# Kernel tuning notes

Measured on AMD Instinct MI355X. Metric: run time of the kernel, lower is better.

Reference implementation:

```python
import jax, jax.numpy as jnp
import numpy as np

E, H, D = 512, 8, 64
B, T = 2, 1024
HD = H * D


def _linear(x, W, b):
    return x @ W + b


def _ln(x, g, b):
    mu = x.mean(-1, keepdims=True)
    var = ((x - mu) ** 2).mean(-1, keepdims=True)
    return (x - mu) / jnp.sqrt(var + 1e-5) * g + b


def _l2norm(x):
    n = jnp.sqrt((x * x).sum(-1, keepdims=True))
    return x / jnp.maximum(n, 1e-12)


def setup_inputs() -> dict:
    key = jax.random.key(0)
    ks = jax.random.split(key, 32)
    s = 0.02
    inp = {
        'x': jax.random.normal(ks[0], (B, T, E), jnp.float32),
        'b_min': jax.random.normal(ks[1], (B, T, E), jnp.float32),
        'b_max': jax.random.normal(ks[2], (B, T, E), jnp.float32),
        'motif_context': jax.random.normal(ks[3], (B, T, E), jnp.float32),
        'Wk': jax.random.normal(ks[4], (E, HD), jnp.float32) * s,
        'bk': jnp.zeros((HD,), jnp.float32),
        'Wq': jax.random.normal(ks[5], (E, HD), jnp.float32) * s,
        'bq': jnp.zeros((HD,), jnp.float32),
        'Wv': jax.random.normal(ks[6], (E, HD), jnp.float32) * s,
        'bv': jnp.zeros((HD,), jnp.float32),
        'Wo': jax.random.normal(ks[7], (HD, E), jnp.float32) * s,
        'bo': jnp.zeros((E,), jnp.float32),
        'Wd': jax.random.normal(ks[8], (E, H), jnp.float32) * s,
        'bd': jnp.zeros((H,), jnp.float32),
        'Wgw': jax.random.normal(ks[9], (E, H), jnp.float32) * s,
        'bgw': jnp.zeros((H,), jnp.float32),
        'Wgf': jax.random.normal(ks[10], (E, H), jnp.float32) * s,
        'bgf': jnp.zeros((H,), jnp.float32),
        'Wps': jax.random.normal(ks[11], (E, E), jnp.float32) * s,
        'bps': jnp.zeros((E,), jnp.float32),
        'ln1_g': jnp.ones((E,), jnp.float32),
        'ln1_b': jnp.zeros((E,), jnp.float32),
        'ln2_g': jnp.ones((E,), jnp.float32),
        'ln2_b': jnp.zeros((E,), jnp.float32),
        'W1': jax.random.normal(ks[12], (E, 4 * E), jnp.float32) * s,
        'b1': jnp.zeros((4 * E,), jnp.float32),
        'W2': jax.random.normal(ks[13], (4 * E, E), jnp.float32) * s,
        'b2': jnp.zeros((E,), jnp.float32),
    }
    return inp


def reference(x, b_min, b_max, motif_context,
              Wk, bk, Wq, bq, Wv, bv, Wo, bo, Wd, bd,
              Wgw, bgw, Wgf, bgf, Wps, bps,
              ln1_g, ln1_b, ln2_g, ln2_b, W1, b1, W2, b2):
    Bs, Ts, Es = x.shape
    x_n = _ln(x, ln1_g, ln1_b)
    k = _l2norm(_linear(x_n, Wk, bk).reshape(Bs, Ts, H, D))
    q = _l2norm(_linear(x_n, Wq, bq).reshape(Bs, Ts, H, D))
    v = jnp.tanh(_linear(x_n, Wv, bv).reshape(Bs, Ts, H, D))
    d = jax.nn.softplus(_linear(x_n, Wd, bd))            # (B,T,H)
    gw = jax.nn.sigmoid(_linear(x_n, Wgw, bgw)) ** 2     # (B,T,H)
    gf = 1.0 - jax.nn.sigmoid(_linear(x_n, Wgf, bgf)) ** 2

    # gated linear recurrent scan via cumsum of rank-1 updates
    v_gated = v * (d * gw)[..., None]                    # (B,T,H,D)
    updates = jnp.einsum('bthi,bthj->bthij', v_gated, k)  # (B,T,H,D,D)
    decay = jnp.clip(d * gf, 1e-6, 0.999)
    log_decay = jnp.log(decay)[..., None, None]          # (B,T,H,1,1)
    exp_cum_decay = jnp.exp(jnp.cumsum(log_decay, axis=1))
    state = jnp.cumsum(updates / (exp_cum_decay + 1e-8), axis=1) * exp_cum_decay
    readout = jnp.einsum('bthij,bthj->bthi', state, q)   # (B,T,H,D)
    next_mem = state[:, -1]

    x2 = x + _linear(readout.reshape(Bs, Ts, HD), Wo, bo) + 0.1 * motif_context
    h = _ln(x2, ln2_g, ln2_b)
    x3 = x2 + _linear(jax.nn.gelu(_linear(h, W1, b1), approximate=False), W2, b2)
    probe = _linear(x3, Wps, bps)
    return (x3, next_mem, b_min + probe, b_max + probe)
```

## Files before the change

kernel.cpp:

```cpp
#include <hip/hip_runtime.h>


typedef unsigned short u16;
typedef unsigned int u32;
typedef __attribute__((ext_vector_type(8))) short short8;
typedef __attribute__((ext_vector_type(4))) float floatx4;

__device__ __forceinline__ float b2f(u16 u) {
  u32 x = ((u32)u) << 16;
  return __uint_as_float(x);
}
__device__ __forceinline__ u16 f2b(float f) {
  u32 x = __float_as_uint(f);
  u32 r = (x + 0x7fffu + ((x >> 16) & 1u)) >> 16;
  return (u16)r;
}
__device__ __forceinline__ float4 b4_to_f4(uint2 u) {
  float4 r;
  r.x = __uint_as_float((u.x & 0xffffu) << 16);
  r.y = __uint_as_float(u.x & 0xffff0000u);
  r.z = __uint_as_float((u.y & 0xffffu) << 16);
  r.w = __uint_as_float(u.y & 0xffff0000u);
  return r;
}

__device__ __forceinline__ void stage16(const u16* g, u16* lds_wave_base) {
  __builtin_amdgcn_global_load_lds((const __attribute__((address_space(1))) void*)g,
                                   (__attribute__((address_space(3))) void*)lds_wave_base,
                                   16, 0, 0);
}

template <int ROWS>
__device__ __forceinline__ void stage_tile64(const u16* __restrict__ G, int ldK, int kb,
                                             u16* lds, int tid) {
#pragma unroll
  for (int r = 0; r < ROWS / 32; ++r) {
    int slot = r * 256 + tid;
    int row = slot >> 3;
    int kwg = (slot & 7) ^ (row & 7);
    stage16(G + (size_t)row * ldK + kb * 64 + kwg * 8,
            lds + (size_t)(r * 256 + (tid >> 6) * 64) * 8);
  }
}

__device__ __forceinline__ void ln_row(const float* __restrict__ xr,
                                       const float* __restrict__ g,
                                       const float* __restrict__ bt,
                                       u16* __restrict__ yr, int tid, float* red) {
  float x0 = xr[tid], x1 = xr[tid + 256];
  float s = x0 + x1, ss = x0 * x0 + x1 * x1;
#pragma unroll
  for (int o = 32; o > 0; o >>= 1) { s += __shfl_xor(s, o); ss += __shfl_xor(ss, o); }
  if ((tid & 63) == 0) { red[tid >> 6] = s; red[4 + (tid >> 6)] = ss; }
  __syncthreads();
  float ts = red[0] + red[1] + red[2] + red[3];
  float tss = red[4] + red[5] + red[6] + red[7];
  float mu = ts * (1.f / 512.f);
  float var = tss * (1.f / 512.f) - mu * mu;
  float rstd = 1.0f / sqrtf(var + 1e-5f);
  yr[tid] = f2b((x0 - mu) * rstd * g[tid] + bt[tid]);
  yr[tid + 256] = f2b((x1 - mu) * rstd * g[tid + 256] + bt[tid + 256]);
}

__global__ __launch_bounds__(256) void prep_weights(
    const float* __restrict__ Wk, const float* __restrict__ Wq,
    const float* __restrict__ Wv, const float* __restrict__ Wo,
    const float* __restrict__ Wps, const float* __restrict__ W1,
    const float* __restrict__ W2, const float* __restrict__ Wd,
    const float* __restrict__ Wgw, const float* __restrict__ Wgf,
    const float* __restrict__ bk, const float* __restrict__ bq,
    const float* __restrict__ bv, const float* __restrict__ bd,
    const float* __restrict__ bgw, const float* __restrict__ bgf,
    const float* __restrict__ x, const float* __restrict__ ln1g,
    const float* __restrict__ ln1b,
    u16* __restrict__ WTQ, u16* __restrict__ WTO, u16* __restrict__ WTPS,
    u16* __restrict__ WT1, u16* __restrict__ WT2, float* __restrict__ BQV,
    u16* __restrict__ XN) {
  int bid = blockIdx.x, tid = threadIdx.x;
  __shared__ float tile[32][33];
  __shared__ float red[8];
#pragma unroll 1
  for (int rep = 0; rep < 3; ++rep) {
    __syncthreads();
    if (bid < 3328) {
      const float* src;
      u16* dst;
      int C, rel, tiles_x;
      if (bid < 256)       { src = Wk;  dst = WTQ;           C = 512;  rel = bid;        tiles_x = 16; }
      else if (bid < 512)  { src = Wq;  dst = WTQ + 262144;  C = 512;  rel = bid - 256;  tiles_x = 16; }
      else if (bid < 768)  { src = Wv;  dst = WTQ + 524288;  C = 512;  rel = bid - 512;  tiles_x = 16; }
      else if (bid < 1024) { src = Wo;  dst = WTO;           C = 512;  rel = bid - 768;  tiles_x = 16; }
      else if (bid < 1280) { src = Wps; dst = WTPS;          C = 512;  rel = bid - 1024; tiles_x = 16; }
      else if (bid < 2304) { src = W1;  dst = WT1;           C = 2048; rel = bid - 1280; tiles_x = 64; }
      else                 { src = W2;  dst = WT2;           C = 512;  rel = bid - 2304; tiles_x = 16; }
      int R = (bid >= 1280 && bid < 2304) ? 512 : (bid >= 2304 ? 2048 : 512);
      int c0 = (rel % tiles_x) * 32, r0 = (rel / tiles_x) * 32;
      int tx = tid & 31, ty = tid >> 5;
#pragma unroll
      for (int i = 0; i < 4; ++i)
        tile[ty + i * 8][tx] = src[(size_t)(r0 + ty + i * 8) * C + c0 + tx];
      __syncthreads();
#pragma unroll
      for (int i = 0; i < 4; ++i)
        dst[(size_t)(c0 + ty + i * 8) * R + r0 + tx] = f2b(tile[tx][ty + i * 8]);
    } else if (bid < 3392) {
      int idx = (bid - 3328) * 256 + tid;
      const int stride = 64 * 256;
      for (int i = idx; i < 128 * 512; i += stride) {
        int local = i >> 9, k = i & 511;
        float v = 0.f;
        if (local < 8) v = Wd[k * 8 + local];
        else if (local < 16) v = Wgw[k * 8 + (local - 8)];
        else if (local < 24) v = Wgf[k * 8 + (local - 16)];
        WTQ[(size_t)(1536 + local) * 512 + k] = f2b(v);
      }
      for (int i = idx; i < 1664; i += stride) {
        float v = 0.f;
        if (i < 512) v = bk[i];
        else if (i < 1024) v = bq[i - 512];
        else if (i < 1536) v = bv[i - 1024];
        else if (i < 1544) v = bd[i - 1536];
        else if (i < 1552) v = bgw[i - 1544];
        else if (i < 1560) v = bgf[i - 1552];
        BQV[i] = v;
      }
    } else {
      int row = bid - 3392;
      ln_row(x + (size_t)row * 512, ln1g, ln1b, XN + (size_t)row * 512, tid, red);
    }
  }
}

__global__ __launch_bounds__(256) void ln_f32(const float* __restrict__ X,
                                              const float* __restrict__ g,
                                              const float* __restrict__ bt,
                                              u16* __restrict__ Y) {
  __shared__ float red[8];
#pragma unroll 1
  for (int rep = 0; rep < 3; ++rep) {
    __syncthreads();
    ln_row(X + (size_t)blockIdx.x * 512, g, bt, Y + (size_t)blockIdx.x * 512,
           threadIdx.x, red);
  }
}

template <int BM, int EPI>
__global__ __launch_bounds__(256, 4) void gemm2s(
    const u16* __restrict__ A, const u16* __restrict__ BT, const float* __restrict__ bias,
    float* __restrict__ outf, float* __restrict__ outf2, u16* __restrict__ outb,
    u16* __restrict__ outb2, u16* __restrict__ outb3,
    const float* __restrict__ aux0, const float* __restrict__ aux1, int M, int N, int K) {
  constexpr int MT = BM / 32;
  constexpr int S = BM / 32 + 2;
  constexpr int STAGES = (BM == 32 ? 3 : 2);
  __shared__ __align__(16) u16 As[STAGES][BM * 64];
  __shared__ __align__(16) u16 Bs[STAGES][64 * 64];
  __shared__ float ssb[2][BM];
  const int tid = threadIdx.x;
  const int lane = tid & 63, wave = tid >> 6;
  const int wm = wave >> 1, wn = wave & 1;
  const int m0 = blockIdx.y * BM, n0 = blockIdx.x * 64;
  floatx4 acc[MT][2] = {};
  const int fr = lane & 15, kq = lane >> 4;
  const int nk = K >> 6;
  const u16* Ab = A + (size_t)m0 * K;
  const u16* Bb = BT + (size_t)n0 * K;

  stage_tile64<BM>(Ab, K, 0, As[0], tid);
  stage_tile64<64>(Bb, K, 0, Bs[0], tid);
  if constexpr (STAGES == 3) {
    if (nk > 1) {
      stage_tile64<BM>(Ab, K, 1, As[1], tid);
      stage_tile64<64>(Bb, K, 1, Bs[1], tid);
    }
  }

  for (int kb = 0; kb < nk; ++kb) {
    const int cur = kb % STAGES;
    if (kb + STAGES - 1 < nk) {
      const int nxt = (kb + STAGES - 1) % STAGES;
      stage_tile64<BM>(Ab, K, kb + STAGES - 1, As[nxt], tid);
      stage_tile64<64>(Bb, K, kb + STAGES - 1, Bs[nxt], tid);
    }
    if constexpr (STAGES == 3) {
      if (kb + 2 < nk) asm volatile("s_waitcnt vmcnt(6)" ::: "memory");
      else if (kb + 1 < nk) asm volatile("s_waitcnt vmcnt(3)" ::: "memory");
      else asm volatile("s_waitcnt vmcnt(0)" ::: "memory");
    } else {
      if (kb + 1 < nk) {
        if constexpr (S == 4) asm volatile("s_waitcnt vmcnt(4)" ::: "memory");
        else asm volatile("s_waitcnt vmcnt(3)" ::: "memory");
      } else {
        asm volatile("s_waitcnt vmcnt(0)" ::: "memory");
      }
    }
    asm volatile("s_barrier" ::: "memory");

#pragma unroll
    for (int sub = 0; sub < 2; ++sub) {
      short8 af[MT], bf[2];
#pragma unroll
      for (int mt = 0; mt < MT; ++mt) {
        int row = wm * (BM / 2) + mt * 16 + fr;
        int c = sub * 4 + kq;
        af[mt] = *(const short8*)&As[cur][row * 64 + ((c ^ (row & 7)) << 3)];
      }
#pragma unroll
      for (int nt = 0; nt < 2; ++nt) {
        int row = wn * 32 + nt * 16 + fr;
        int c = sub * 4 + kq;
        bf[nt] = *(const short8*)&Bs[cur][row * 64 + ((c ^ (row & 7)) << 3)];
      }
#pragma unroll
      for (int mt = 0; mt < MT; ++mt)
#pragma unroll
        for (int nt = 0; nt < 2; ++nt)
          acc[mt][nt] =
              __builtin_amdgcn_mfma_f32_16x16x32_bf16(af[mt], bf[nt], acc[mt][nt], 0, 0, 0);
    }
    asm volatile("s_waitcnt lgkmcnt(0)" ::: "memory");
    asm volatile("s_barrier" ::: "memory");
  }

  const int col = lane & 15;
  const int rbase = (lane >> 4) * 4;

  float vv[MT][2][4];
#pragma unroll
  for (int nt = 0; nt < 2; ++nt) {
    int gc = n0 + wn * 32 + nt * 16 + col;
    float bvv = bias[gc];
#pragma unroll
    for (int mt = 0; mt < MT; ++mt)
#pragma unroll
      for (int r = 0; r < 4; ++r) vv[mt][nt][r] = acc[mt][nt][r] + bvv;
  }

  if constexpr (EPI == 5) {
    const int sec = n0 >> 9;
    const int h = (n0 & 511) >> 6;
    if (sec == 3) {
#pragma unroll
      for (int nt = 0; nt < 2; ++nt) {
        int gcl = (n0 - 1536) + wn * 32 + nt * 16 + col;
#pragma unroll
        for (int mt = 0; mt < MT; ++mt) {
          int gr = m0 + wm * (BM / 2) + mt * 16 + rbase;
#pragma unroll
          for (int r = 0; r < 4; ++r)
            outf[(size_t)(gr + r) * 128 + gcl] = vv[mt][nt][r];
        }
      }
    } else if (sec == 2) {
#pragma unroll
      for (int nt = 0; nt < 2; ++nt) {
        int d = wn * 32 + nt * 16 + col;
#pragma unroll
        for (int mt = 0; mt < MT; ++mt) {
          int gr = m0 + wm * (BM / 2) + mt * 16 + rbase;
#pragma unroll
          for (int r = 0; r < 4; ++r) {
            int tok = gr + r;
            int bh = (tok >> 10) * 8 + h;
            outb3[((size_t)bh * 1024 + (tok & 1023)) * 64 + d] = f2b(tanhf(vv[mt][nt][r]));
          }
        }
      }
    } else {
#pragma unroll
      for (int mt = 0; mt < MT; ++mt) {
#pragma unroll
        for (int r = 0; r < 4; ++r) {
          float ss = vv[mt][0][r] * vv[mt][0][r] + vv[mt][1][r] * vv[mt][1][r];
          ss += __shfl_xor(ss, 1);
          ss += __shfl_xor(ss, 2);
          ss += __shfl_xor(ss, 4);
          ss += __shfl_xor(ss, 8);
          if ((lane & 15) == 0)
            ssb[wn][wm * (BM / 2) + mt * 16 + rbase + r] = ss;
        }
      }
      __syncthreads();
      u16* dst = (sec == 0) ? outb : outb2;
#pragma unroll
      for (int mt = 0; mt < MT; ++mt) {
#pragma unroll
        for (int r = 0; r < 4; ++r) {
          int br = wm * (BM / 2) + mt * 16 + rbase + r;
          float tot = ssb[0][br] + ssb[1][br];
          float rs = 1.0f / fmaxf(sqrtf(tot), 1e-12f);
          int tok = m0 + br;
          int bh = (tok >> 10) * 8 + h;
          size_t base = ((size_t)bh * 1024 + (tok & 1023)) * 64;
#pragma unroll
          for (int nt = 0; nt < 2; ++nt) {
            int d = wn * 32 + nt * 16 + col;
            dst[base + d] = f2b(vv[mt][nt][r] * rs);
          }
        }
      }
    }
  } else {
#pragma unroll
    for (int nt = 0; nt < 2; ++nt) {
      int gc = n0 + wn * 32 + nt * 16 + col;
#pragma unroll
      for (int mt = 0; mt < MT; ++mt) {
        int gr = m0 + wm * (BM / 2) + mt * 16 + rbase;
#pragma unroll
        for (int r = 0; r < 4; ++r) {
          size_t idx = (size_t)(gr + r) * N + gc;
          float v = vv[mt][nt][r];
          if constexpr (EPI == 1) {
            outf[idx] = aux0[idx] + v + 0.1f * aux1[idx];
          } else if constexpr (EPI == 2) {
            outb[idx] = f2b(0.5f * v * (1.f + erff(v * 0.70710678118654752f)));
          } else if constexpr (EPI == 3) {
            float w = aux0[idx] + v;
            outf[idx] = w;
            outb[idx] = f2b(w);
          } else if constexpr (EPI == 4) {
            outf[idx] = aux0[idx] + v;
            outf2[idx] = aux1[idx] + v;
          }
        }
      }
    }
  }
}

__global__ __launch_bounds__(256) void gates_logcum(
    const float* __restrict__ G0, float* __restrict__ DEC, float* __restrict__ WS,
    float* __restrict__ LC) {
  int bh = blockIdx.x;
  int b = bh >> 3, h = bh & 7;
  int tid = threadIdx.x;
  __shared__ float ldec[1024];
  __shared__ float lsvg[1024];
#pragma unroll 1
  for (int rep = 0; rep < 3; ++rep) {
    __syncthreads();
#pragma unroll
    for (int tt = 0; tt < 4; ++tt) {
      int t = tt * 256 + tid;
      size_t tok = (size_t)b * 1024 + t;
      float dl = G0[tok * 128 + h];
      float gwl = G0[tok * 128 + 8 + h];
      float gfl = G0[tok * 128 + 16 + h];
      float dd = dl > 20.f ? dl : log1pf(expf(dl));
      float sw = 1.f / (1.f + expf(-gwl));
      float gw = sw * sw;
      float sf = 1.f / (1.f + expf(-gfl));
      float gf = 1.f - sf * sf;
      float dec = fminf(fmaxf(dd * gf, 1e-6f), 0.999f);
      ldec[t] = dec;
      lsvg[t] = dd * gw;
      DEC[(size_t)bh * 1024 + t] = dec;
    }
    __syncthreads();
    if (tid < 64) {
      int lane = tid;
      size_t base = (size_t)bh * 1024 + lane * 16;
      float loc[16];
      float run = 0.f;
#pragma unroll
      for (int i = 0; i < 16; ++i) { run += logf(ldec[lane * 16 + i]); loc[i] = run; }
      float x = run;
#pragma unroll
      for (int o = 1; o < 64; o <<= 1) {
        float v = __shfl_up(x, o);
        if (lane >= o) x += v;
      }
      float excl = x - run;
#pragma unroll
      for (int i = 0; i < 16; ++i) {
        float L = excl + loc[i];
        LC[base + i] = L;
        float c = expf(L);
        WS[base + i] = (c / (c + 1e-8f)) * lsvg[lane * 16 + i];
      }
    }
  }
}

__global__ __launch_bounds__(256, 2) void scan_phase1(
    const u16* __restrict__ KB, const u16* __restrict__ QB, const u16* __restrict__ VB,
    const float* __restrict__ DEC, const float* __restrict__ WS,
    float* __restrict__ RP, float* __restrict__ SF) {
  int chunk = blockIdx.x, h = blockIdx.y, b = blockIdx.z;
  int bh = b * 8 + h;
  int t0 = chunk * 32;
  __shared__ __align__(16) float sk[2048], sq[2048], sv[2048];
  __shared__ float lsa[32], lsw[32];
  int tid = threadIdx.x;

#pragma unroll 1
  for (int rep = 0; rep < 3; ++rep) {
    __syncthreads();
    const u16* gk = KB + ((size_t)bh * 1024 + t0) * 64;
    const u16* gq = QB + ((size_t)bh * 1024 + t0) * 64;
    const u16* gv = VB + ((size_t)bh * 1024 + t0) * 64;
#pragma unroll
    for (int r = 0; r < 2; ++r) {
      int f = (r * 256 + tid) * 4;
      *(float4*)&sk[f] = b4_to_f4(*(const uint2*)(gk + f));
      *(float4*)&sq[f] = b4_to_f4(*(const uint2*)(gq + f));
      *(float4*)&sv[f] = b4_to_f4(*(const uint2*)(gv + f));
    }
    if (tid < 32) {
      size_t gi = (size_t)bh * 1024 + t0 + tid;
      lsa[tid] = DEC[gi];
      lsw[tid] = WS[gi];
    }
    __syncthreads();

    int i = tid >> 2, j0 = (tid & 3) * 16;
    float s[16];
#pragma unroll
    for (int z = 0; z < 16; ++z) s[z] = 0.f;

    for (int t = 0; t < 32; ++t) {
      float a = lsa[t], w = lsw[t];
      float wv = w * sv[t * 64 + i];
      float r = 0.f;
#pragma unroll
      for (int u4 = 0; u4 < 4; ++u4) {
        float4 kv = *(const float4*)&sk[t * 64 + j0 + u4 * 4];
        float4 qv = *(const float4*)&sq[t * 64 + j0 + u4 * 4];
        s[u4 * 4 + 0] = fmaf(a, s[u4 * 4 + 0], wv * kv.x); r = fmaf(s[u4 * 4 + 0], qv.x, r);
        s[u4 * 4 + 1] = fmaf(a, s[u4 * 4 + 1], wv * kv.y); r = fmaf(s[u4 * 4 + 1], qv.y, r);
        s[u4 * 4 + 2] = fmaf(a, s[u4 * 4 + 2], wv * kv.z); r = fmaf(s[u4 * 4 + 2], qv.z, r);
        s[u4 * 4 + 3] = fmaf(a, s[u4 * 4 + 3], wv * kv.w); r = fmaf(s[u4 * 4 + 3], qv.w, r);
      }
      r += __shfl_xor(r, 1);
      r += __shfl_xor(r, 2);
      if ((tid & 3) == 0)
        RP[((size_t)(b * 1024 + t0 + t) * 8 + h) * 64 + i] = r;
    }

    float* Sf = SF + ((size_t)bh * 32 + chunk) * 4096 + i * 64 + j0;
#pragma unroll
    for (int u4 = 0; u4 < 4; ++u4) {
      float4 v;
      v.x = s[u4 * 4 + 0]; v.y = s[u4 * 4 + 1]; v.z = s[u4 * 4 + 2]; v.w = s[u4 * 4 + 3];
      *(float4*)&Sf[u4 * 4] = v;
    }
  }
}

__global__ __launch_bounds__(256) void scan_phase2p(const float* __restrict__ SF,
                                                    const float* __restrict__ LC,
                                                    float* __restrict__ SI,
                                                    float* __restrict__ next_mem) {
  int bh = blockIdx.x >> 4;
  int e = (blockIdx.x & 15) * 256 + threadIdx.x;
#pragma unroll 1
  for (int rep = 0; rep < 3; ++rep) {
    float s = 0.f;
    for (int c = 0; c < 32; ++c) {
      SI[((size_t)bh * 32 + c) * 4096 + e] = s;
      float Lend = LC[(size_t)bh * 1024 + c * 32 + 31];
      float Lpre = c ? LC[(size_t)bh * 1024 + c * 32 - 1] : 0.f;
      float P = expf(Lend - Lpre);
      s = fmaf(P, s, SF[((size_t)bh * 32 + c) * 4096 + e]);
    }
    next_mem[(size_t)bh * 4096 + e] = s;
  }
}

__global__ __launch_bounds__(256, 2) void scan_phase3(
    const u16* __restrict__ QB, const float* __restrict__ SI, const float* __restrict__ LC,
    const float* __restrict__ RP, u16* __restrict__ AB) {
  int chunk = blockIdx.x, h = blockIdx.y, b = blockIdx.z;
  int bh = b * 8 + h;
  int t0 = chunk * 32;
  __shared__ __align__(16) float sq[2048];
  __shared__ float sL[32];
  int tid = threadIdx.x;

#pragma unroll 1
  for (int rep = 0; rep < 3; ++rep) {
    __syncthreads();
    const u16* gq = QB + ((size_t)bh * 1024 + t0) * 64;
#pragma unroll
    for (int r = 0; r < 2; ++r) {
      int f = (r * 256 + tid) * 4;
      *(float4*)&sq[f] = b4_to_f4(*(const uint2*)(gq + f));
    }
    if (tid < 32) sL[tid] = LC[(size_t)bh * 1024 + t0 + tid];
    __syncthreads();

    float Lpre = chunk ? LC[(size_t)bh * 1024 + t0 - 1] : 0.f;
    int i = tid >> 2, j0 = (tid & 3) * 16;
    const float* Si = SI + ((size_t)bh * 32 + chunk) * 4096 + i * 64 + j0;
    float S[16];
#pragma unroll
    for (int u4 = 0; u4 < 4; ++u4) {
      float4 v = *(const float4*)&Si[u4 * 4];
      S[u4 * 4 + 0] = v.x; S[u4 * 4 + 1] = v.y; S[u4 * 4 + 2] = v.z; S[u4 * 4 + 3] = v.w;
    }

    for (int t = 0; t < 32; ++t) {
      float p = expf(sL[t] - Lpre);
      float r = 0.f;
#pragma unroll
      for (int u4 = 0; u4 < 4; ++u4) {
        float4 qv = *(const float4*)&sq[t * 64 + j0 + u4 * 4];
        r = fmaf(S[u4 * 4 + 0], qv.x, r);
        r = fmaf(S[u4 * 4 + 1], qv.y, r);
        r = fmaf(S[u4 * 4 + 2], qv.z, r);
        r = fmaf(S[u4 * 4 + 3], qv.w, r);
      }
      r += __shfl_xor(r, 1);
      r += __shfl_xor(r, 2);
      if ((tid & 3) == 0) {
        size_t gi = ((size_t)(b * 1024 + t0 + t) * 8 + h) * 64 + i;
        AB[gi] = f2b(RP[gi] + p * r);
      }
    }
  }
}

extern "C" void kernel_launch(void* const* d_in, const int* in_sizes, int n_in,
                              void* d_out, int out_size, void* d_ws, size_t ws_size,
                              hipStream_t stream) {
  const float* x = (const float*)d_in[0];
  const float* bmin = (const float*)d_in[1];
  const float* bmax = (const float*)d_in[2];
  const float* motif = (const float*)d_in[3];
  const float* Wk = (const float*)d_in[4];
  const float* bk = (const float*)d_in[5];
  const float* Wq = (const float*)d_in[6];
  const float* bq = (const float*)d_in[7];
  const float* Wv = (const float*)d_in[8];
  const float* bv = (const float*)d_in[9];
  const float* Wo = (const float*)d_in[10];
  const float* bo = (const float*)d_in[11];
  const float* Wd = (const float*)d_in[12];
  const float* bd = (const float*)d_in[13];
  const float* Wgw = (const float*)d_in[14];
  const float* bgw = (const float*)d_in[15];
  const float* Wgf = (const float*)d_in[16];
  const float* bgf = (const float*)d_in[17];
  const float* Wps = (const float*)d_in[18];
  const float* bps = (const float*)d_in[19];
  const float* ln1g = (const float*)d_in[20];
  const float* ln1b = (const float*)d_in[21];
  const float* ln2g = (const float*)d_in[22];
  const float* ln2b = (const float*)d_in[23];
  const float* W1 = (const float*)d_in[24];
  const float* b1 = (const float*)d_in[25];
  const float* W2 = (const float*)d_in[26];
  const float* b2 = (const float*)d_in[27];

  char* ws = (char*)d_ws;
  u16* WTQ = (u16*)(ws + 0);
  u16* WTO = (u16*)(ws + 1703936);
  u16* WT1 = (u16*)(ws + 2228224);
  u16* WT2 = (u16*)(ws + 4325376);
  u16* WTPS = (u16*)(ws + 6422528);
  float* BQV = (float*)(ws + 6946816);
  u16* XN = (u16*)(ws + 6953984);
  float* G0 = (float*)(ws + 9051136);
  u16* KB = (u16*)(ws + 10099712);
  u16* QB = (u16*)(ws + 12196864);
  u16* VB = (u16*)(ws + 14294016);
  float* DEC = (float*)(ws + 16391168);
  float* LC = (float*)(ws + 16456704);
  float* WS = (float*)(ws + 16522240);
  float* RP = (float*)(ws + 16653312);
  float* SF = (float*)(ws + 20847616);
  float* SI = (float*)(ws + 29236224);
  u16* AB = (u16*)(ws + 37624832);
  float* X2 = (float*)(ws + 39721984);
  u16* HB = (u16*)(ws + 43916288);
  u16* MID = (u16*)(ws + 9051136);
  u16* X3B = (u16*)(ws + 20847616);

  float* out0 = (float*)d_out;
  float* out1 = out0 + 1048576;
  float* out2 = out0 + 1114112;
  float* out3 = out0 + 2162688;

  prep_weights<<<5440, 256, 0, stream>>>(Wk, Wq, Wv, Wo, Wps, W1, W2, Wd, Wgw, Wgf,
                                         bk, bq, bv, bd, bgw, bgf, x, ln1g, ln1b,
                                         WTQ, WTO, WTPS, WT1, WT2, BQV, XN);
  gemm2s<64, 5><<<dim3(26, 32), 256, 0, stream>>>(XN, WTQ, BQV, G0, nullptr, KB, QB, VB,
                                                  nullptr, nullptr, 2048, 1664, 512);
  gates_logcum<<<16, 256, 0, stream>>>(G0, DEC, WS, LC);
  scan_phase1<<<dim3(32, 8, 2), 256, 0, stream>>>(KB, QB, VB, DEC, WS, RP, SF);
  scan_phase2p<<<256, 256, 0, stream>>>(SF, LC, SI, out1);
  scan_phase3<<<dim3(32, 8, 2), 256, 0, stream>>>(QB, SI, LC, RP, AB);

  gemm2s<32, 1><<<dim3(8, 64), 256, 0, stream>>>(AB, WTO, bo, X2, nullptr, nullptr,
                                                 nullptr, nullptr, x, motif, 2048, 512, 512);
  ln_f32<<<2048, 256, 0, stream>>>(X2, ln2g, ln2b, HB);
  gemm2s<64, 2><<<dim3(32, 32), 256, 0, stream>>>(HB, WT1, b1, nullptr, nullptr, MID,
                                                  nullptr, nullptr, nullptr, nullptr,
                                                  2048, 2048, 512);
  gemm2s<32, 3><<<dim3(8, 64), 256, 0, stream>>>(MID, WT2, b2, out0, nullptr, X3B,
                                                 nullptr, nullptr, X2, nullptr,
                                                 2048, 512, 2048);
  gemm2s<32, 4><<<dim3(8, 64), 256, 0, stream>>>(X3B, WTPS, bps, out2, out3, nullptr,
                                                 nullptr, nullptr, bmin, bmax,
                                                 2048, 512, 512);
}
```

Before: 279.6 us.

## Fold LN2 into W1 GEMM epilogue and drop redundant repeat loops

Removes the standalone ln_f32 kernel. The Wo GEMM epilogue now writes x2 in both fp32 and bf16 and accumulates per-row sum and sum-of-squares with atomics. The W1 GEMM applies the normalisation algebraically, using ln2_g folded into the transposed W1 and precomputed column vectors U1 and V1. It also deletes the triple-repeat loops in the prep, gates, scan and LN kernels, which redid identical work three times. The trade-offs are atomics in the epilogue, a variance computed as E[x^2]-mu^2, and GEMM input that is x2 rounded to bf16 before normalisation instead of after.

```diff
diff --git a/kernel.cpp b/kernel.cpp
--- a/kernel.cpp
+++ b/kernel.cpp
@@ -72,75 +72,74 @@
     const float* __restrict__ bv, const float* __restrict__ bd,
     const float* __restrict__ bgw, const float* __restrict__ bgf,
     const float* __restrict__ x, const float* __restrict__ ln1g,
-    const float* __restrict__ ln1b,
+    const float* __restrict__ ln1b, const float* __restrict__ ln2g,
+    const float* __restrict__ ln2b, const float* __restrict__ b1v,
     u16* __restrict__ WTQ, u16* __restrict__ WTO, u16* __restrict__ WTPS,
     u16* __restrict__ WT1, u16* __restrict__ WT2, float* __restrict__ BQV,
-    u16* __restrict__ XN) {
+    u16* __restrict__ XN, float* __restrict__ U1, float* __restrict__ V1,
+    float* __restrict__ RS) {
   int bid = blockIdx.x, tid = threadIdx.x;
   __shared__ float tile[32][33];
   __shared__ float red[8];
-#pragma unroll 1
-  for (int rep = 0; rep < 3; ++rep) {
+  if (bid < 3328) {
+    const float* src;
+    u16* dst;
+    int C, rel, tiles_x;
+    bool foldg = (bid >= 1280 && bid < 2304);
+    if (bid < 256)       { src = Wk;  dst = WTQ;           C = 512;  rel = bid;        tiles_x = 16; }
+    else if (bid < 512)  { src = Wq;  dst = WTQ + 262144;  C = 512;  rel = bid - 256;  tiles_x = 16; }
+    else if (bid < 768)  { src = Wv;  dst = WTQ + 524288;  C = 512;  rel = bid - 512;  tiles_x = 16; }
+    else if (bid < 1024) { src = Wo;  dst = WTO;           C = 512;  rel = bid - 768;  tiles_x = 16; }
+    else if (bid < 1280) { src = Wps; dst = WTPS;          C = 512;  rel = bid - 1024; tiles_x = 16; }
+    else if (bid < 2304) { src = W1;  dst = WT1;           C = 2048; rel = bid - 1280; tiles_x = 64; }
+    else                 { src = W2;  dst = WT2;           C = 512;  rel = bid - 2304; tiles_x = 16; }
+    int R = foldg ? 512 : (bid >= 2304 ? 2048 : 512);
+    int c0 = (rel % tiles_x) * 32, r0 = (rel / tiles_x) * 32;
+    int tx = tid & 31, ty = tid >> 5;
+#pragma unroll
+    for (int i = 0; i < 4; ++i)
+      tile[ty + i * 8][tx] = src[(size_t)(r0 + ty + i * 8) * C + c0 + tx];
     __syncthreads();
-    if (bid < 3328) {
-      const float* src;
-      u16* dst;
-      int C, rel, tiles_x;
-      if (bid < 256)       { src = Wk;  dst = WTQ;           C = 512;  rel = bid;        tiles_x = 16; }
-      else if (bid < 512)  { src = Wq;  dst = WTQ + 262144;  C = 512;  rel = bid - 256;  tiles_x = 16; }
-      else if (bid < 768)  { src = Wv;  dst = WTQ + 524288;  C = 512;  rel = bid - 512;  tiles_x = 16; }
-      else if (bid < 1024) { src = Wo;  dst = WTO;           C = 512;  rel = bid - 768;  tiles_x = 16; }
-      else if (bid < 1280) { src = Wps; dst = WTPS;          C = 512;  rel = bid - 1024; tiles_x = 16; }
-      else if (bid < 2304) { src = W1;  dst = WT1;           C = 2048; rel = bid - 1280; tiles_x = 64; }
-      else                 { src = W2;  dst = WT2;           C = 512;  rel = bid - 2304; tiles_x = 16; }
-      int R = (bid >= 1280 && bid < 2304) ? 512 : (bid >= 2304 ? 2048 : 512);
-      int c0 = (rel % tiles_x) * 32, r0 = (rel / tiles_x) * 32;
-      int tx = tid & 31, ty = tid >> 5;
-#pragma unroll
-      for (int i = 0; i < 4; ++i)
-        tile[ty + i * 8][tx] = src[(size_t)(r0 + ty + i * 8) * C + c0 + tx];
-      __syncthreads();
-#pragma unroll
-      for (int i = 0; i < 4; ++i)
-        dst[(size_t)(c0 + ty + i * 8) * R + r0 + tx] = f2b(tile[tx][ty + i * 8]);
-    } else if (bid < 3392) {
-      int idx = (bid - 3328) * 256 + tid;
-      const int stride = 64 * 256;
-      for (int i = idx; i < 128 * 512; i += stride) {
-        int local = i >> 9, k = i & 511;
-        float v = 0.f;
-        if (local < 8) v = Wd[k * 8 + local];
-        else if (local < 16) v = Wgw[k * 8 + (local - 8)];
-        else if (local < 24) v = Wgf[k * 8 + (local - 16)];
-        WTQ[(size_t)(1536 + local) * 512 + k] = f2b(v);
-      }
-      for (int i = idx; i < 1664; i += stride) {
-        float v = 0.f;
-        if (i < 512) v = bk[i];
-        else if (i < 1024) v = bq[i - 512];
-        else if (i < 1536) v = bv[i - 1024];
-        else if (i < 1544) v = bd[i - 1536];
-        else if (i < 1552) v = bgw[i - 1544];
-        else if (i < 1560) v = bgf[i - 1552];
-        BQV[i] = v;
-      }
-    } else {
-      int row = bid - 3392;
-      ln_row(x + (size_t)row * 512, ln1g, ln1b, XN + (size_t)row * 512, tid, red);
-    }
-  }
-}
-
-__global__ __launch_bounds__(256) void ln_f32(const float* __restrict__ X,
-                                              const float* __restrict__ g,
-                                              const float* __restrict__ bt,
-                                              u16* __restrict__ Y) {
-  __shared__ float red[8];
-#pragma unroll 1
-  for (int rep = 0; rep < 3; ++rep) {
-    __syncthreads();
-    ln_row(X + (size_t)blockIdx.x * 512, g, bt, Y + (size_t)blockIdx.x * 512,
-           threadIdx.x, red);
+    float gs = foldg ? ln2g[r0 + tx] : 1.f;
+#pragma unroll
+    for (int i = 0; i < 4; ++i)
+      dst[(size_t)(c0 + ty + i * 8) * R + r0 + tx] = f2b(gs * tile[tx][ty + i * 8]);
+  } else if (bid < 3392) {
+    int idx = (bid - 3328) * 256 + tid;
+    const int stride = 64 * 256;
+    for (int i = idx; i < 128 * 512; i += stride) {
+      int local = i >> 9, k = i & 511;
+      float v = 0.f;
+      if (local < 8) v = Wd[k * 8 + local];
+      else if (local < 16) v = Wgw[k * 8 + (local - 8)];
+      else if (local < 24) v = Wgf[k * 8 + (local - 16)];
+      WTQ[(size_t)(1536 + local) * 512 + k] = f2b(v);
+    }
+    for (int i = idx; i < 1664; i += stride) {
+      float v = 0.f;
+      if (i < 512) v = bk[i];
+      else if (i < 1024) v = bq[i - 512];
+      else if (i < 1536) v = bv[i - 1024];
+      else if (i < 1544) v = bd[i - 1536];
+      else if (i < 1552) v = bgw[i - 1544];
+      else if (i < 1560) v = bgf[i - 1552];
+      BQV[i] = v;
+    }
+  } else if (bid < 5440) {
+    int row = bid - 3392;
+    ln_row(x + (size_t)row * 512, ln1g, ln1b, XN + (size_t)row * 512, tid, red);
+  } else {
+    int c = (bid - 5440) * 256 + tid;
+    float u = 0.f, vv = 0.f;
+    for (int k = 0; k < 512; ++k) {
+      float w = W1[(size_t)k * 2048 + c];
+      u = fmaf(ln2g[k], w, u);
+      vv = fmaf(ln2b[k], w, vv);
+    }
+    U1[c] = u;
+    V1[c] = vv + b1v[c];
+    RS[2 * c] = 0.f;
+    RS[2 * c + 1] = 0.f;
   }
 }
 
@@ -229,7 +228,9 @@
 #pragma unroll
   for (int nt = 0; nt < 2; ++nt) {
     int gc = n0 + wn * 32 + nt * 16 + col;
-    float bvv = bias[gc];
+    float bvv;
+    if constexpr (EPI == 7) bvv = 0.f;
+    else bvv = bias[gc];
 #pragma unroll
     for (int mt = 0; mt < MT; ++mt)
 #pragma unroll
@@ -300,6 +301,52 @@
         }
       }
     }
+  } else if constexpr (EPI == 6) {
+#pragma unroll
+    for (int mt = 0; mt < MT; ++mt) {
+#pragma unroll
+      for (int r = 0; r < 4; ++r) {
+        int gr = m0 + wm * (BM / 2) + mt * 16 + rbase + r;
+        float s = 0.f, ss2 = 0.f;
+#pragma unroll
+        for (int nt = 0; nt < 2; ++nt) {
+          int gc = n0 + wn * 32 + nt * 16 + col;
+          size_t idx = (size_t)gr * N + gc;
+          float w = aux0[idx] + vv[mt][nt][r] + 0.1f * aux1[idx];
+          outf[idx] = w;
+          outb[idx] = f2b(w);
+          s += w;
+          ss2 += w * w;
+        }
+        s += __shfl_xor(s, 1); ss2 += __shfl_xor(ss2, 1);
+        s += __shfl_xor(s, 2); ss2 += __shfl_xor(ss2, 2);
+        s += __shfl_xor(s, 4); ss2 += __shfl_xor(ss2, 4);
+        s += __shfl_xor(s, 8); ss2 += __shfl_xor(ss2, 8);
+        if ((lane & 15) == 0) {
+          atomicAdd(&outf2[2 * gr], s);
+          atomicAdd(&outf2[2 * gr + 1], ss2);
+        }
+      }
+    }
+  } else if constexpr (EPI == 7) {
+#pragma unroll
+    for (int mt = 0; mt < MT; ++mt) {
+#pragma unroll
+      for (int r = 0; r < 4; ++r) {
+        int gr = m0 + wm * (BM / 2) + mt * 16 + rbase + r;
+        float sum = outf[2 * gr], ssq = outf[2 * gr + 1];
+        float mu = sum * (1.f / 512.f);
+        float var = ssq * (1.f / 512.f) - mu * mu;
+        float rstd = 1.0f / sqrtf(var + 1e-5f);
+#pragma unroll
+        for (int nt = 0; nt < 2; ++nt) {
+          int gc = n0 + wn * 32 + nt * 16 + col;
+          float y = rstd * vv[mt][nt][r] - rstd * mu * aux0[gc] + aux1[gc];
+          float g = 0.5f * y * (1.f + erff(y * 0.70710678118654752f));
+          outb[(size_t)gr * N + gc] = f2b(g);
+        }
+      }
+    }
   } else {
 #pragma unroll
     for (int nt = 0; nt < 2; ++nt) {
@@ -311,11 +358,7 @@
         for (int r = 0; r < 4; ++r) {
           size_t idx = (size_t)(gr + r) * N + gc;
           float v = vv[mt][nt][r];
-          if constexpr (EPI == 1) {
-            outf[idx] = aux0[idx] + v + 0.1f * aux1[idx];
-          } else if constexpr (EPI == 2) {
-            outb[idx] = f2b(0.5f * v * (1.f + erff(v * 0.70710678118654752f)));
-          } else if constexpr (EPI == 3) {
+          if constexpr (EPI == 3) {
             float w = aux0[idx] + v;
             outf[idx] = w;
             outb[idx] = f2b(w);
@@ -337,48 +380,44 @@
   int tid = threadIdx.x;
   __shared__ float ldec[1024];
   __shared__ float lsvg[1024];
-#pragma unroll 1
-  for (int rep = 0; rep < 3; ++rep) {
-    __syncthreads();
-#pragma unroll
-    for (int tt = 0; tt < 4; ++tt) {
-      int t = tt * 256 + tid;
-      size_t tok = (size_t)b * 1024 + t;
-      float dl = G0[tok * 128 + h];
-      float gwl = G0[tok * 128 + 8 + h];
-      float gfl = G0[tok * 128 + 16 + h];
-      float dd = dl > 20.f ? dl : log1pf(expf(dl));
-      float sw = 1.f / (1.f + expf(-gwl));
-      float gw = sw * sw;
-      float sf = 1.f / (1.f + expf(-gfl));
-      float gf = 1.f - sf * sf;
-      float dec = fminf(fmaxf(dd * gf, 1e-6f), 0.999f);
-      ldec[t] = dec;
-      lsvg[t] = dd * gw;
-      DEC[(size_t)bh * 1024 + t] = dec;
-    }
-    __syncthreads();
-    if (tid < 64) {
-      int lane = tid;
-      size_t base = (size_t)bh * 1024 + lane * 16;
-      float loc[16];
-      float run = 0.f;
-#pragma unroll
-      for (int i = 0; i < 16; ++i) { run += logf(ldec[lane * 16 + i]); loc[i] = run; }
-      float x = run;
-#pragma unroll
-      for (int o = 1; o < 64; o <<= 1) {
-        float v = __shfl_up(x, o);
-        if (lane >= o) x += v;
-      }
-      float excl = x - run;
-#pragma unroll
-      for (int i = 0; i < 16; ++i) {
-        float L = excl + loc[i];
-        LC[base + i] = L;
-        float c = expf(L);
-        WS[base + i] = (c / (c + 1e-8f)) * lsvg[lane * 16 + i];
-      }
+#pragma unroll
+  for (int tt = 0; tt < 4; ++tt) {
+    int t = tt * 256 + tid;
+    size_t tok = (size_t)b * 1024 + t;
+    float dl = G0[tok * 128 + h];
+    float gwl = G0[tok * 128 + 8 + h];
+    float gfl = G0[tok * 128 + 16 + h];
+    float dd = dl > 20.f ? dl : log1pf(expf(dl));
+    float sw = 1.f / (1.f + expf(-gwl));
+    float gw = sw * sw;
+    float sf = 1.f / (1.f + expf(-gfl));
+    float gf = 1.f - sf * sf;
+    float dec = fminf(fmaxf(dd * gf, 1e-6f), 0.999f);
+    ldec[t] = dec;
+    lsvg[t] = dd * gw;
+    DEC[(size_t)bh * 1024 + t] = dec;
+  }
+  __syncthreads();
+  if (tid < 64) {
+    int lane = tid;
+    size_t base = (size_t)bh * 1024 + lane * 16;
+    float loc[16];
+    float run = 0.f;
+#pragma unroll
+    for (int i = 0; i < 16; ++i) { run += logf(ldec[lane * 16 + i]); loc[i] = run; }
+    float x = run;
+#pragma unroll
+    for (int o = 1; o < 64; o <<= 1) {
+      float v = __shfl_up(x, o);
+      if (lane >= o) x += v;
+    }
+    float excl = x - run;
+#pragma unroll
+    for (int i = 0; i < 16; ++i) {
+      float L = excl + loc[i];
+      LC[base + i] = L;
+      float c = expf(L);
+      WS[base + i] = (c / (c + 1e-8f)) * lsvg[lane * 16 + i];
     }
   }
 }
@@ -394,57 +433,53 @@
   __shared__ float lsa[32], lsw[32];
   int tid = threadIdx.x;
 
-#pragma unroll 1
-  for (int rep = 0; rep < 3; ++rep) {
-    __syncthreads();
-    const u16* gk = KB + ((size_t)bh * 1024 + t0) * 64;
-    const u16* gq = QB + ((size_t)bh * 1024 + t0) * 64;
-    const u16* gv = VB + ((size_t)bh * 1024 + t0) * 64;
-#pragma unroll
-    for (int r = 0; r < 2; ++r) {
-      int f = (r * 256 + tid) * 4;
-      *(float4*)&sk[f] = b4_to_f4(*(const uint2*)(gk + f));
-      *(float4*)&sq[f] = b4_to_f4(*(const uint2*)(gq + f));
-      *(float4*)&sv[f] = b4_to_f4(*(const uint2*)(gv + f));
-    }
-    if (tid < 32) {
-      size_t gi = (size_t)bh * 1024 + t0 + tid;
-      lsa[tid] = DEC[gi];
-      lsw[tid] = WS[gi];
-    }
-    __syncthreads();
-
-    int i = tid >> 2, j0 = (tid & 3) * 16;
-    float s[16];
-#pragma unroll
-    for (int z = 0; z < 16; ++z) s[z] = 0.f;
-
-    for (int t = 0; t < 32; ++t) {
-      float a = lsa[t], w = lsw[t];
-      float wv = w * sv[t * 64 + i];
-      float r = 0.f;
-#pragma unroll
-      for (int u4 = 0; u4 < 4; ++u4) {
-        float4 kv = *(const float4*)&sk[t * 64 + j0 + u4 * 4];
-        float4 qv = *(const float4*)&sq[t * 64 + j0 + u4 * 4];
-        s[u4 * 4 + 0] = fmaf(a, s[u4 * 4 + 0], wv * kv.x); r = fmaf(s[u4 * 4 + 0], qv.x, r);
-        s[u4 * 4 + 1] = fmaf(a, s[u4 * 4 + 1], wv * kv.y); r = fmaf(s[u4 * 4 + 1], qv.y, r);
-        s[u4 * 4 + 2] = fmaf(a, s[u4 * 4 + 2], wv * kv.z); r = fmaf(s[u4 * 4 + 2], qv.z, r);
-        s[u4 * 4 + 3] = fmaf(a, s[u4 * 4 + 3], wv * kv.w); r = fmaf(s[u4 * 4 + 3], qv.w, r);
-      }
-      r += __shfl_xor(r, 1);
-      r += __shfl_xor(r, 2);
-      if ((tid & 3) == 0)
-        RP[((size_t)(b * 1024 + t0 + t) * 8 + h) * 64 + i] = r;
-    }
-
-    float* Sf = SF + ((size_t)bh * 32 + chunk) * 4096 + i * 64 + j0;
+  const u16* gk = KB + ((size_t)bh * 1024 + t0) * 64;
+  const u16* gq = QB + ((size_t)bh * 1024 + t0) * 64;
+  const u16* gv = VB + ((size_t)bh * 1024 + t0) * 64;
+#pragma unroll
+  for (int r = 0; r < 2; ++r) {
+    int f = (r * 256 + tid) * 4;
+    *(float4*)&sk[f] = b4_to_f4(*(const uint2*)(gk + f));
+    *(float4*)&sq[f] = b4_to_f4(*(const uint2*)(gq + f));
+    *(float4*)&sv[f] = b4_to_f4(*(const uint2*)(gv + f));
+  }
+  if (tid < 32) {
+    size_t gi = (size_t)bh * 1024 + t0 + tid;
+    lsa[tid] = DEC[gi];
+    lsw[tid] = WS[gi];
+  }
+  __syncthreads();
+
+  int i = tid >> 2, j0 = (tid & 3) * 16;
+  float s[16];
+#pragma unroll
+  for (int z = 0; z < 16; ++z) s[z] = 0.f;
+
+  for (int t = 0; t < 32; ++t) {
+    float a = lsa[t], w = lsw[t];
+    float wv = w * sv[t * 64 + i];
+    float r = 0.f;
 #pragma unroll
     for (int u4 = 0; u4 < 4; ++u4) {
-      float4 v;
-      v.x = s[u4 * 4 + 0]; v.y = s[u4 * 4 + 1]; v.z = s[u4 * 4 + 2]; v.w = s[u4 * 4 + 3];
-      *(float4*)&Sf[u4 * 4] = v;
-    }
+      float4 kv = *(const float4*)&sk[t * 64 + j0 + u4 * 4];
+      float4 qv = *(const float4*)&sq[t * 64 + j0 + u4 * 4];
+      s[u4 * 4 + 0] = fmaf(a, s[u4 * 4 + 0], wv * kv.x); r = fmaf(s[u4 * 4 + 0], qv.x, r);
+      s[u4 * 4 + 1] = fmaf(a, s[u4 * 4 + 1], wv * kv.y); r = fmaf(s[u4 * 4 + 1], qv.y, r);
+      s[u4 * 4 + 2] = fmaf(a, s[u4 * 4 + 2], wv * kv.z); r = fmaf(s[u4 * 4 + 2], qv.z, r);
+      s[u4 * 4 + 3] = fmaf(a, s[u4 * 4 + 3], wv * kv.w); r = fmaf(s[u4 * 4 + 3], qv.w, r);
+    }
+    r += __shfl_xor(r, 1);
+    r += __shfl_xor(r, 2);
+    if ((tid & 3) == 0)
+      RP[((size_t)(b * 1024 + t0 + t) * 8 + h) * 64 + i] = r;
+  }
+
+  float* Sf = SF + ((size_t)bh * 32 + chunk) * 4096 + i * 64 + j0;
+#pragma unroll
+  for (int u4 = 0; u4 < 4; ++u4) {
+    float4 v;
+    v.x = s[u4 * 4 + 0]; v.y = s[u4 * 4 + 1]; v.z = s[u4 * 4 + 2]; v.w = s[u4 * 4 + 3];
+    *(float4*)&Sf[u4 * 4] = v;
   }
 }
 
@@ -454,18 +489,15 @@
                                                     float* __restrict__ next_mem) {
   int bh = blockIdx.x >> 4;
   int e = (blockIdx.x & 15) * 256 + threadIdx.x;
-#pragma unroll 1
-  for (int rep = 0; rep < 3; ++rep) {
-    float s = 0.f;
-    for (int c = 0; c < 32; ++c) {
-      SI[((size_t)bh * 32 + c) * 4096 + e] = s;
-      float Lend = LC[(size_t)bh * 1024 + c * 32 + 31];
-      float Lpre = c ? LC[(size_t)bh * 1024 + c * 32 - 1] : 0.f;
-      float P = expf(Lend - Lpre);
-      s = fmaf(P, s, SF[((size_t)bh * 32 + c) * 4096 + e]);
-    }
-    next_mem[(size_t)bh * 4096 + e] = s;
-  }
+  float s = 0.f;
+  for (int c = 0; c < 32; ++c) {
+    SI[((size_t)bh * 32 + c) * 4096 + e] = s;
+    float Lend = LC[(size_t)bh * 1024 + c * 32 + 31];
+    float Lpre = c ? LC[(size_t)bh * 1024 + c * 32 - 1] : 0.f;
+    float P = expf(Lend - Lpre);
+    s = fmaf(P, s, SF[((size_t)bh * 32 + c) * 4096 + e]);
+  }
+  next_mem[(size_t)bh * 4096 + e] = s;
 }
 
 __global__ __launch_bounds__(256, 2) void scan_phase3(
@@ -478,45 +510,41 @@
   __shared__ float sL[32];
   int tid = threadIdx.x;
 
-#pragma unroll 1
-  for (int rep = 0; rep < 3; ++rep) {
-    __syncthreads();
-    const u16* gq = QB + ((size_t)bh * 1024 + t0) * 64;
-#pragma unroll
-    for (int r = 0; r < 2; ++r) {
-      int f = (r * 256 + tid) * 4;
-      *(float4*)&sq[f] = b4_to_f4(*(const uint2*)(gq + f));
-    }
-    if (tid < 32) sL[tid] = LC[(size_t)bh * 1024 + t0 + tid];
-    __syncthreads();
-
-    float Lpre = chunk ? LC[(size_t)bh * 1024 + t0 - 1] : 0.f;
-    int i = tid >> 2, j0 = (tid & 3) * 16;
-    const float* Si = SI + ((size_t)bh * 32 + chunk) * 4096 + i * 64 + j0;
-    float S[16];
+  const u16* gq = QB + ((size_t)bh * 1024 + t0) * 64;
+#pragma unroll
+  for (int r = 0; r < 2; ++r) {
+    int f = (r * 256 + tid) * 4;
+    *(float4*)&sq[f] = b4_to_f4(*(const uint2*)(gq + f));
+  }
+  if (tid < 32) sL[tid] = LC[(size_t)bh * 1024 + t0 + tid];
+  __syncthreads();
+
+  float Lpre = chunk ? LC[(size_t)bh * 1024 + t0 - 1] : 0.f;
+  int i = tid >> 2, j0 = (tid & 3) * 16;
+  const float* Si = SI + ((size_t)bh * 32 + chunk) * 4096 + i * 64 + j0;
+  float S[16];
+#pragma unroll
+  for (int u4 = 0; u4 < 4; ++u4) {
+    float4 v = *(const float4*)&Si[u4 * 4];
+    S[u4 * 4 + 0] = v.x; S[u4 * 4 + 1] = v.y; S[u4 * 4 + 2] = v.z; S[u4 * 4 + 3] = v.w;
+  }
+
+  for (int t = 0; t < 32; ++t) {
+    float p = expf(sL[t] - Lpre);
+    float r = 0.f;
 #pragma unroll
     for (int u4 = 0; u4 < 4; ++u4) {
-      float4 v = *(const float4*)&Si[u4 * 4];
-      S[u4 * 4 + 0] = v.x; S[u4 * 4 + 1] = v.y; S[u4 * 4 + 2] = v.z; S[u4 * 4 + 3] = v.w;
-    }
-
-    for (int t = 0; t < 32; ++t) {
-      float p = expf(sL[t] - Lpre);
-      float r = 0.f;
-#pragma unroll
-      for (int u4 = 0; u4 < 4; ++u4) {
-        float4 qv = *(const float4*)&sq[t * 64 + j0 + u4 * 4];
-        r = fmaf(S[u4 * 4 + 0], qv.x, r);
-        r = fmaf(S[u4 * 4 + 1], qv.y, r);
-        r = fmaf(S[u4 * 4 + 2], qv.z, r);
-        r = fmaf(S[u4 * 4 + 3], qv.w, r);
-      }
-      r += __shfl_xor(r, 1);
-      r += __shfl_xor(r, 2);
-      if ((tid & 3) == 0) {
-        size_t gi = ((size_t)(b * 1024 + t0 + t) * 8 + h) * 64 + i;
-        AB[gi] = f2b(RP[gi] + p * r);
-      }
+      float4 qv = *(const float4*)&sq[t * 64 + j0 + u4 * 4];
+      r = fmaf(S[u4 * 4 + 0], qv.x, r);
+      r = fmaf(S[u4 * 4 + 1], qv.y, r);
+      r = fmaf(S[u4 * 4 + 2], qv.z, r);
+      r = fmaf(S[u4 * 4 + 3], qv.w, r);
+    }
+    r += __shfl_xor(r, 1);
+    r += __shfl_xor(r, 2);
+    if ((tid & 3) == 0) {
+      size_t gi = ((size_t)(b * 1024 + t0 + t) * 8 + h) * 64 + i;
+      AB[gi] = f2b(RP[gi] + p * r);
     }
   }
 }
@@ -573,7 +601,10 @@
   float* SI = (float*)(ws + 29236224);
   u16* AB = (u16*)(ws + 37624832);
   float* X2 = (float*)(ws + 39721984);
-  u16* HB = (u16*)(ws + 43916288);
+  u16* XB2 = (u16*)(ws + 43916288);
+  float* U1 = (float*)(ws + 46013440);
+  float* V1 = (float*)(ws + 46021632);
+  float* RS = (float*)(ws + 46029824);
   u16* MID = (u16*)(ws + 9051136);
   u16* X3B = (u16*)(ws + 20847616);
 
@@ -582,9 +613,10 @@
   float* out2 = out0 + 1114112;
   float* out3 = out0 + 2162688;
 
-  prep_weights<<<5440, 256, 0, stream>>>(Wk, Wq, Wv, Wo, Wps, W1, W2, Wd, Wgw, Wgf,
+  prep_weights<<<5448, 256, 0, stream>>>(Wk, Wq, Wv, Wo, Wps, W1, W2, Wd, Wgw, Wgf,
                                          bk, bq, bv, bd, bgw, bgf, x, ln1g, ln1b,
-                                         WTQ, WTO, WTPS, WT1, WT2, BQV, XN);
+                                         ln2g, ln2b, b1,
+                                         WTQ, WTO, WTPS, WT1, WT2, BQV, XN, U1, V1, RS);
   gemm2s<64, 5><<<dim3(26, 32), 256, 0, stream>>>(XN, WTQ, BQV, G0, nullptr, KB, QB, VB,
                                                   nullptr, nullptr, 2048, 1664, 512);
   gates_logcum<<<16, 256, 0, stream>>>(G0, DEC, WS, LC);
@@ -592,11 +624,10 @@
   scan_phase2p<<<256, 256, 0, stream>>>(SF, LC, SI, out1);
   scan_phase3<<<dim3(32, 8, 2), 256, 0, stream>>>(QB, SI, LC, RP, AB);
 
-  gemm2s<32, 1><<<dim3(8, 64), 256, 0, stream>>>(AB, WTO, bo, X2, nullptr, nullptr,
+  gemm2s<32, 6><<<dim3(8, 64), 256, 0, stream>>>(AB, WTO, bo, X2, RS, XB2,
                                                  nullptr, nullptr, x, motif, 2048, 512, 512);
-  ln_f32<<<2048, 256, 0, stream>>>(X2, ln2g, ln2b, HB);
-  gemm2s<64, 2><<<dim3(32, 32), 256, 0, stream>>>(HB, WT1, b1, nullptr, nullptr, MID,
-                                                  nullptr, nullptr, nullptr, nullptr,
+  gemm2s<64, 7><<<dim3(32, 32), 256, 0, stream>>>(XB2, WT1, b1, RS, nullptr, MID,
+                                                  nullptr, nullptr, U1, V1,
                                                   2048, 2048, 512);
   gemm2s<32, 3><<<dim3(8, 64), 256, 0, stream>>>(MID, WT2, b2, out0, nullptr, X3B,
                                                  nullptr, nullptr, X2, nullptr,
```

Measured after the change: 253.9 us. -9.2%, faster.
